# Kernel tuning notes

Measured on AMD Instinct MI355X. Metric: run time of the kernel, lower is better.

Reference implementation:

```python
import jax, jax.numpy as jnp
import numpy as np

NUM_HEADS = 16
ROPE_THETA = 10000.0


def _rope_tables(S, d_k):
    # angles[s, j] = s / theta^(2j/d_k), j over d_k/2 pairs
    inv_freq = 1.0 / (ROPE_THETA ** (jnp.arange(0, d_k, 2, dtype=jnp.float32) / d_k))
    angles = jnp.arange(S, dtype=jnp.float32)[:, None] * inv_freq[None, :]  # [S, d_k/2]
    # repeat_interleave(…, 2, dim=-1) -> [S, d_k]
    cos2 = jnp.repeat(jnp.cos(angles), 2, axis=-1)
    sin2 = jnp.repeat(jnp.sin(angles), 2, axis=-1)
    return cos2, sin2


def _rotate_half(x):
    x_even = x[..., 0::2]
    x_odd = x[..., 1::2]
    return jnp.stack([-x_odd, x_even], axis=-1).reshape(x.shape)


def _apply_rope(x, cos2, sin2):
    # x: [B, H, S, d_k]; cos2/sin2: [S, d_k] broadcast over B, H
    return x * cos2 + _rotate_half(x) * sin2


def setup_inputs() -> dict:
    key = jax.random.key(0)
    k1, k2, k3, k4, k5 = jax.random.split(key, 5)
    B, S, D = 2, 2048, 1024
    std = (2.0 / (D + D)) ** 0.5
    x = jax.random.normal(k1, (B, S, D), dtype=jnp.float32)
    Wq = jax.random.normal(k2, (D, D), dtype=jnp.float32) * std
    Wk = jax.random.normal(k3, (D, D), dtype=jnp.float32) * std
    Wv = jax.random.normal(k4, (D, D), dtype=jnp.float32) * std
    Wo = jax.random.normal(k5, (D, D), dtype=jnp.float32) * std
    return {"x": x, "Wq": Wq, "Wk": Wk, "Wv": Wv, "Wo": Wo}


def reference(x, Wq, Wk, Wv, Wo):
    B, S, D = x.shape
    H = NUM_HEADS
    d_k = D // H
    # Linear is y = W x with W[d_out, d_in]
    Q = jnp.einsum('bsd,ed->bse', x, Wq).reshape(B, S, H, d_k).transpose(0, 2, 1, 3)
    K = jnp.einsum('bsd,ed->bse', x, Wk).reshape(B, S, H, d_k).transpose(0, 2, 1, 3)
    V = jnp.einsum('bsd,ed->bse', x, Wv).reshape(B, S, H, d_k).transpose(0, 2, 1, 3)
    cos2, sin2 = _rope_tables(S, d_k)
    Q = _apply_rope(Q, cos2, sin2)
    K = _apply_rope(K, cos2, sin2)
    scores = jnp.einsum('bhqd,bhkd->bhqk', Q, K) / jnp.sqrt(jnp.float32(d_k))
    causal = jnp.tril(jnp.ones((S, S), dtype=bool))
    scores = jnp.where(causal, scores, -jnp.inf)
    attn = jax.nn.softmax(scores, axis=-1)
    out = jnp.einsum('bhqk,bhkd->bhqd', attn, V)  # [B,H,S,d_k]
    out = out.transpose(0, 2, 1, 3).reshape(B, S, D)
    return jnp.einsum('bsd,ed->bse', out, Wo)
```

## Files before the change

### kernel.cpp

```cpp
#include <hip/hip_runtime.h>
#include <hip/hip_bf16.h>

typedef float f32x4 __attribute__((ext_vector_type(4)));
typedef __bf16 bf16x8 __attribute__((ext_vector_type(8)));

static constexpr int S  = 2048;
static constexpr int D  = 1024;
static constexpr int DK = 64;
static constexpr int KDIM = 1024;

#define AS1 __attribute__((address_space(1)))
#define AS3 __attribute__((address_space(3)))

__device__ __forceinline__ void glds16(const void* g, void* l) {
  __builtin_amdgcn_global_load_lds((const AS1 void*)g, (AS3 void*)l, 16, 0, 0);
}

__device__ __forceinline__ unsigned cvtpk(float lo, float hi) {
  unsigned r;
  asm("v_cvt_pk_bf16_f32 %0, %1, %2" : "=v"(r) : "v"(lo), "v"(hi));
  return r;
}

__device__ __forceinline__ void pl32swap(unsigned& a, unsigned& b) {
  asm("v_permlane32_swap_b32 %0, %1" : "+v"(a), "+v"(b));
}

__device__ __forceinline__ int kperm64(int k) {
  const int kf = k >> 4, hs = (k >> 2) & 3, r = k & 3;
  const bool inl = ((kf & 1) == (hs >> 1));
  const int h = inl ? hs : (hs ^ 2);
  const int j = inl ? r : (r + 4);
  return ((kf >> 1) << 5) + (h << 3) + j;
}

__global__ __launch_bounds__(256) void cvt4_kernel(const float* __restrict__ src,
                                                   __hip_bfloat16* __restrict__ dst,
                                                   int n4) {
  int i = blockIdx.x * 256 + threadIdx.x;
  if (i >= n4) return;
  float4 v = reinterpret_cast<const float4*>(src)[i];
  union { ushort4 u; __hip_bfloat16 h[4]; } o;
  o.h[0] = __float2bfloat16(v.x);
  o.h[1] = __float2bfloat16(v.y);
  o.h[2] = __float2bfloat16(v.z);
  o.h[3] = __float2bfloat16(v.w);
  reinterpret_cast<ushort4*>(dst)[i] = o.u;
}

__global__ __launch_bounds__(256) void rope_tab_kernel(float* __restrict__ cosT,
                                                       float* __restrict__ sinT) {
  int idx = blockIdx.x * 256 + threadIdx.x;
  int s = idx >> 5, fi = idx & 31;
  float invf = powf(10000.0f, -(float)(2 * fi) / 64.0f);
  float ang = (float)s * invf;
  cosT[idx] = cosf(ang);
  sinT[idx] = sinf(ang);
}

template <int MODE>
__global__ __launch_bounds__(256) void gemm_nt_kernel(
    const __hip_bfloat16* __restrict__ A,
    const __hip_bfloat16* __restrict__ Bw,
    float* __restrict__ Cf,
    __hip_bfloat16* __restrict__ Qr,
    __hip_bfloat16* __restrict__ Kr,
    __hip_bfloat16* __restrict__ Vt,
    const float* __restrict__ cosT,
    const float* __restrict__ sinT,
    int Ncols) {
  __shared__ __attribute__((aligned(16))) __hip_bfloat16 Asm[128 * 32];
  __shared__ __attribute__((aligned(16))) __hip_bfloat16 Bsm[128 * 32];
  const int tid = threadIdx.x;
  const int nbn = Ncols >> 7;
  const int bm = blockIdx.x / nbn;
  const int bn = blockIdx.x % nbn;
  const int m0 = bm << 7, n0 = bn << 7;
  const int lane = tid & 63;
  const int wid = tid >> 6;
  const int wm = wid >> 1, wn = wid & 1;
  const int r16 = lane & 15, hf = lane >> 4;

  f32x4 acc[4][4];
#pragma unroll
  for (int i = 0; i < 4; ++i)
#pragma unroll
    for (int j = 0; j < 4; ++j) acc[i][j] = (f32x4)0.0f;

  for (int k0 = 0; k0 < KDIM; k0 += 32) {
    __syncthreads();
#pragma unroll
    for (int i = 0; i < 2; ++i) {
      const int idx = i * 256 + tid;
      const int row = idx >> 2;
      const int cb = (idx & 3) << 4;
      glds16((const char*)A + ((size_t)(m0 + row) * KDIM + k0) * 2 + cb,
             (char*)Asm + idx * 16);
      glds16((const char*)Bw + ((size_t)(n0 + row) * KDIM + k0) * 2 + cb,
             (char*)Bsm + idx * 16);
    }
    __syncthreads();
    bf16x8 af[4], bfr[4];
#pragma unroll
    for (int mi = 0; mi < 4; ++mi)
      af[mi] = *(const bf16x8*)((const char*)Asm +
                                ((wm << 6) + (mi << 4) + r16) * 64 + hf * 16);
#pragma unroll
    for (int ni = 0; ni < 4; ++ni)
      bfr[ni] = *(const bf16x8*)((const char*)Bsm +
                                 ((wn << 6) + (ni << 4) + r16) * 64 + hf * 16);
#pragma unroll
    for (int mi = 0; mi < 4; ++mi)
#pragma unroll
      for (int ni = 0; ni < 4; ++ni)
        acc[mi][ni] = __builtin_amdgcn_mfma_f32_16x16x32_bf16(af[mi], bfr[ni],
                                                              acc[mi][ni], 0, 0, 0);
  }

  if constexpr (MODE == 0) {
#pragma unroll
    for (int mi = 0; mi < 4; ++mi) {
      const int rowb = m0 + (wm << 6) + (mi << 4) + (hf << 2);
#pragma unroll
      for (int ni = 0; ni < 4; ++ni) {
        const int col = n0 + (wn << 6) + (ni << 4) + r16;
#pragma unroll
        for (int r = 0; r < 4; ++r)
          Cf[(size_t)(rowb + r) * Ncols + col] = acc[mi][ni][r];
      }
    }
  } else {
    const int proj = n0 >> 10;
#pragma unroll
    for (int mi = 0; mi < 4; ++mi) {
      const int rowb = m0 + (wm << 6) + (mi << 4) + (hf << 2);
#pragma unroll
      for (int ni = 0; ni < 4; ++ni) {
        const int col = n0 + (wn << 6) + (ni << 4) + r16;
        const int ecol = col & 1023;
        const int h = ecol >> 6, dk = ecol & 63;
#pragma unroll
        for (int r = 0; r < 4; ++r) {
          float v = acc[mi][ni][r];
          const int row = rowb + r;
          const int b = row >> 11, s = row & 2047;
          if (proj < 2) {
            float p = __shfl_xor(v, 1, 64);
            const int fi = dk >> 1;
            const float c = cosT[(s << 5) + fi];
            const float sn = sinT[(s << 5) + fi];
            const float ov = v * c + ((dk & 1) ? p : -p) * sn;
            __hip_bfloat16* dst = (proj == 0) ? Qr : Kr;
            dst[((size_t)((b << 4) + h) * S + s) * DK + dk] = __float2bfloat16(ov);
          } else {
            const int sp = (s & ~63) | kperm64(s & 63);
            Vt[((size_t)((b << 4) + h) * DK + dk) * S + sp] = __float2bfloat16(v);
          }
        }
      }
    }
  }
}

__global__ __launch_bounds__(256) void attn_kernel(
    const __hip_bfloat16* __restrict__ Q,
    const __hip_bfloat16* __restrict__ Kr,
    const __hip_bfloat16* __restrict__ Vp,
    __hip_bfloat16* __restrict__ AO) {
  __shared__ __attribute__((aligned(16))) __hip_bfloat16 Ks[2][64 * 64];
  __shared__ __attribute__((aligned(16))) __hip_bfloat16 Vs[2][64 * 64];
  const int tid = threadIdx.x;
  const int lane = tid & 63, wid = tid >> 6;
  const int r16 = lane & 15, hf = lane >> 4;
  const bool hi32 = (lane >= 32);
  const int qt = 15 - (blockIdx.x >> 5);
  const int bh = blockIdx.x & 31;
  const __hip_bfloat16* Qh = Q + (size_t)bh * S * DK;
  const __hip_bfloat16* Kh = Kr + (size_t)bh * S * DK;
  const __hip_bfloat16* Vh = Vp + (size_t)bh * DK * S;

  const int qbase = (qt << 7) + (wid << 5);

  bf16x8 bq[2][2];
#pragma unroll
  for (int qf = 0; qf < 2; ++qf)
#pragma unroll
    for (int ks = 0; ks < 2; ++ks)
      bq[qf][ks] = *(const bf16x8*)(Qh + (size_t)(qbase + (qf << 4) + r16) * DK +
                                    ks * 32 + hf * 8);

  f32x4 o[2][4];
#pragma unroll
  for (int qf = 0; qf < 2; ++qf)
#pragma unroll
    for (int f = 0; f < 4; ++f) o[qf][f] = (f32x4)0.0f;
  float m[2] = {-1e30f, -1e30f}, l[2] = {0.0f, 0.0f};

  const int nt = (qt << 1) + 2;

#define STAGE(bufi, t)                                                         \
  {                                                                            \
    _Pragma("unroll") for (int i = 0; i < 2; ++i) {                            \
      const int idx = i * 256 + tid;                                           \
      const int row = idx >> 3;                                                \
      const int cb = (idx & 7) << 4;                                           \
      const int scb = cb ^ ((row & 7) << 4);                                   \
      glds16((const char*)Kh + ((size_t)(((t) << 6) + row) * DK) * 2 + scb,    \
             (char*)(&Ks[bufi][0]) + idx * 16);                                \
      glds16((const char*)Vh + ((size_t)row * S + ((t) << 6)) * 2 + scb,       \
             (char*)(&Vs[bufi][0]) + idx * 16);                                \
    }                                                                          \
  }

  STAGE(0, 0);
  __syncthreads();

  for (int kt = 0; kt < nt; ++kt) {
    const int cur = kt & 1;
    if (kt + 1 < nt) STAGE(cur ^ 1, kt + 1);

    f32x4 p[2][4];
#pragma unroll
    for (int qf = 0; qf < 2; ++qf)
#pragma unroll
      for (int kf = 0; kf < 4; ++kf) p[qf][kf] = (f32x4)0.0f;
    __builtin_amdgcn_s_setprio(1);
#pragma unroll
    for (int ks = 0; ks < 2; ++ks) {
#pragma unroll
      for (int kf = 0; kf < 4; ++kf) {
        const int krow = (kf << 4) + r16;
        const int cb = (ks << 6) + (hf << 4);
        const bf16x8 ak = *(const bf16x8*)((const char*)(&Ks[cur][0]) +
                                           krow * 128 + (cb ^ ((krow & 7) << 4)));
#pragma unroll
        for (int qf = 0; qf < 2; ++qf)
          p[qf][kf] = __builtin_amdgcn_mfma_f32_16x16x32_bf16(ak, bq[qf][ks],
                                                              p[qf][kf], 0, 0, 0);
      }
    }
    __builtin_amdgcn_s_setprio(0);

    const bool diag = (kt >= (qt << 1));
#pragma unroll
    for (int qf = 0; qf < 2; ++qf) {
      const int qg = qbase + (qf << 4) + r16;
#pragma unroll
      for (int kf = 0; kf < 4; ++kf)
#pragma unroll
        for (int r = 0; r < 4; ++r) {
          float sv = p[qf][kf][r] * 0.125f;
          if (diag) {
            const int kg = (kt << 6) + (kf << 4) + (hf << 2) + r;
            if (kg > qg) sv = -1e30f;
          }
          p[qf][kf][r] = sv;
        }
    }

    float scl[2];
#pragma unroll
    for (int qf = 0; qf < 2; ++qf) {
      float t = p[qf][0][0];
#pragma unroll
      for (int kf = 0; kf < 4; ++kf)
#pragma unroll
        for (int r = 0; r < 4; ++r) t = fmaxf(t, p[qf][kf][r]);
      t = fmaxf(t, __shfl_xor(t, 16, 64));
      t = fmaxf(t, __shfl_xor(t, 32, 64));
      const float mn = fmaxf(m[qf], t);
      scl[qf] = __expf(m[qf] - mn);
      m[qf] = mn;
      float ss = 0.0f;
#pragma unroll
      for (int kf = 0; kf < 4; ++kf)
#pragma unroll
        for (int r = 0; r < 4; ++r) {
          const float e = __expf(p[qf][kf][r] - mn);
          p[qf][kf][r] = e;
          ss += e;
        }
      ss += __shfl_xor(ss, 16, 64);
      ss += __shfl_xor(ss, 32, 64);
      l[qf] = l[qf] * scl[qf] + ss;
#pragma unroll
      for (int f = 0; f < 4; ++f)
#pragma unroll
        for (int r = 0; r < 4; ++r) o[qf][f][r] *= scl[qf];
    }

    union PW { unsigned u[4]; bf16x8 v; };
    PW pb[2][2];
#pragma unroll
    for (int qf = 0; qf < 2; ++qf) {
      unsigned w[4][2];
#pragma unroll
      for (int kf = 0; kf < 4; ++kf) {
        w[kf][0] = cvtpk(p[qf][kf][0], p[qf][kf][1]);
        w[kf][1] = cvtpk(p[qf][kf][2], p[qf][kf][3]);
      }
#pragma unroll
      for (int ks = 0; ks < 2; ++ks) {
        unsigned a0 = w[2 * ks][0], b0 = w[2 * ks + 1][0];
        unsigned a1 = w[2 * ks][1], b1 = w[2 * ks + 1][1];
        pb[qf][ks].u[0] = hi32 ? b0 : a0;
        pb[qf][ks].u[1] = hi32 ? b1 : a1;
        pl32swap(a0, b0);
        pl32swap(a1, b1);
        pb[qf][ks].u[2] = hi32 ? a0 : b0;
        pb[qf][ks].u[3] = hi32 ? a1 : b1;
      }
    }

    __builtin_amdgcn_s_setprio(1);
#pragma unroll
    for (int ks = 0; ks < 2; ++ks) {
#pragma unroll
      for (int f = 0; f < 4; ++f) {
        const int vrow = (f << 4) + r16;
        const int cb = (ks << 6) + (hf << 4);
        const bf16x8 av = *(const bf16x8*)((const char*)(&Vs[cur][0]) +
                                           vrow * 128 + (cb ^ ((vrow & 7) << 4)));
#pragma unroll
        for (int qf = 0; qf < 2; ++qf)
          o[qf][f] = __builtin_amdgcn_mfma_f32_16x16x32_bf16(av, pb[qf][ks].v,
                                                             o[qf][f], 0, 0, 0);
      }
    }
    __builtin_amdgcn_s_setprio(0);

    __syncthreads();
  }
#undef STAGE

  const int b = bh >> 4, h = bh & 15;
#pragma unroll
  for (int qf = 0; qf < 2; ++qf) {
    const float inv = 1.0f / l[qf];
    const int q = qbase + (qf << 4) + r16;
#pragma unroll
    for (int f = 0; f < 4; ++f)
#pragma unroll
      for (int r = 0; r < 4; ++r) {
        const int dv = (f << 4) + (hf << 2) + r;
        AO[((size_t)b * S + q) * D + (h << 6) + dv] =
            __float2bfloat16(o[qf][f][r] * inv);
      }
  }
}

extern "C" void kernel_launch(void* const* d_in, const int* in_sizes, int n_in,
                              void* d_out, int out_size, void* d_ws, size_t ws_size,
                              hipStream_t stream) {
  (void)in_sizes; (void)n_in; (void)out_size; (void)ws_size;
  const float* x  = (const float*)d_in[0];
  const float* Wq = (const float*)d_in[1];
  const float* Wk = (const float*)d_in[2];
  const float* Wv = (const float*)d_in[3];
  const float* Wo = (const float*)d_in[4];
  float* out = (float*)d_out;
  char* ws = (char*)d_ws;
  const size_t MB = (size_t)1 << 20;
  __hip_bfloat16* xb   = (__hip_bfloat16*)(ws);
  __hip_bfloat16* Wcat = (__hip_bfloat16*)(ws + 8 * MB);
  __hip_bfloat16* Wob  = (__hip_bfloat16*)(ws + 14 * MB);
  __hip_bfloat16* Qr   = (__hip_bfloat16*)(ws + 16 * MB);
  __hip_bfloat16* Kr   = (__hip_bfloat16*)(ws + 24 * MB);
  __hip_bfloat16* Vt   = (__hip_bfloat16*)(ws + 32 * MB);
  __hip_bfloat16* AO   = (__hip_bfloat16*)(ws + 40 * MB);
  float* cosT = (float*)(ws + 48 * MB);
  float* sinT = (float*)(ws + 48 * MB + 256 * 1024);

  cvt4_kernel<<<4096, 256, 0, stream>>>(x, xb, (2 * 2048 * 1024) / 4);
  cvt4_kernel<<<1024, 256, 0, stream>>>(Wq, Wcat, (1024 * 1024) / 4);
  cvt4_kernel<<<1024, 256, 0, stream>>>(Wk, Wcat + 1024 * 1024, (1024 * 1024) / 4);
  cvt4_kernel<<<1024, 256, 0, stream>>>(Wv, Wcat + 2 * 1024 * 1024, (1024 * 1024) / 4);
  cvt4_kernel<<<1024, 256, 0, stream>>>(Wo, Wob, (1024 * 1024) / 4);
  rope_tab_kernel<<<(2048 * 32) / 256, 256, 0, stream>>>(cosT, sinT);

  gemm_nt_kernel<1><<<(4096 / 128) * (3072 / 128), 256, 0, stream>>>(
      xb, Wcat, nullptr, Qr, Kr, Vt, cosT, sinT, 3072);
  attn_kernel<<<32 * 16, 256, 0, stream>>>(Qr, Kr, Vt, AO);
  gemm_nt_kernel<0><<<(4096 / 128) * (1024 / 128), 256, 0, stream>>>(
      AO, Wob, out, nullptr, nullptr, nullptr, nullptr, nullptr, 1024);
}
```

Before: 230.6 us.

## Split long causal attention rows across blocks, fuse preprocessing, swizzle GEMM blocks

Attention work is rebalanced. The eight longest query tiles per head have their KV range split into two halves, each run as its own block, and the eight shorter tiles run whole. The split halves write normalized partial outputs plus (m, l) statistics into reused workspace, and a new merge kernel combines them. The goal is to cut the tail imbalance of the causal triangle. The five conversion launches and the RoPE-table launch are fused into one pre kernel to save launch overhead. GEMM block indices are remapped in an XCD-style interleave to improve L2 locality. Risks are the extra launch and partial-output traffic for the merge, and correctness of the merge if m is kept in a scaled domain.

Result: faster. 221.6 us (-3.9%).

```diff
diff --git a/kernel.cpp b/kernel.cpp
--- a/kernel.cpp
+++ b/kernel.cpp
@@ -34,28 +34,38 @@
   return ((kf >> 1) << 5) + (h << 3) + j;
 }
 
-__global__ __launch_bounds__(256) void cvt4_kernel(const float* __restrict__ src,
-                                                   __hip_bfloat16* __restrict__ dst,
-                                                   int n4) {
-  int i = blockIdx.x * 256 + threadIdx.x;
-  if (i >= n4) return;
-  float4 v = reinterpret_cast<const float4*>(src)[i];
-  union { ushort4 u; __hip_bfloat16 h[4]; } o;
-  o.h[0] = __float2bfloat16(v.x);
-  o.h[1] = __float2bfloat16(v.y);
-  o.h[2] = __float2bfloat16(v.z);
-  o.h[3] = __float2bfloat16(v.w);
-  reinterpret_cast<ushort4*>(dst)[i] = o.u;
-}
-
-__global__ __launch_bounds__(256) void rope_tab_kernel(float* __restrict__ cosT,
-                                                       float* __restrict__ sinT) {
-  int idx = blockIdx.x * 256 + threadIdx.x;
-  int s = idx >> 5, fi = idx & 31;
-  float invf = powf(10000.0f, -(float)(2 * fi) / 64.0f);
-  float ang = (float)s * invf;
-  cosT[idx] = cosf(ang);
-  sinT[idx] = sinf(ang);
+__global__ __launch_bounds__(256) void pre_kernel(
+    const float* __restrict__ x,  const float* __restrict__ Wq,
+    const float* __restrict__ Wk, const float* __restrict__ Wv,
+    const float* __restrict__ Wo,
+    __hip_bfloat16* __restrict__ xb, __hip_bfloat16* __restrict__ Wcat,
+    __hip_bfloat16* __restrict__ Wob,
+    float* __restrict__ cosT, float* __restrict__ sinT) {
+  const int gid = blockIdx.x * 256 + threadIdx.x;
+  if (gid < 2097152) {
+    const float* src;
+    __hip_bfloat16* dst;
+    int off;
+    if (gid < 1048576)      { src = x;  dst = xb;                  off = gid; }
+    else if (gid < 1310720) { src = Wq; dst = Wcat;                off = gid - 1048576; }
+    else if (gid < 1572864) { src = Wk; dst = Wcat + 1048576;      off = gid - 1310720; }
+    else if (gid < 1835008) { src = Wv; dst = Wcat + 2097152;      off = gid - 1572864; }
+    else                    { src = Wo; dst = Wob;                 off = gid - 1835008; }
+    float4 v = reinterpret_cast<const float4*>(src)[off];
+    union { ushort4 u; __hip_bfloat16 h[4]; } o;
+    o.h[0] = __float2bfloat16(v.x);
+    o.h[1] = __float2bfloat16(v.y);
+    o.h[2] = __float2bfloat16(v.z);
+    o.h[3] = __float2bfloat16(v.w);
+    reinterpret_cast<ushort4*>(dst)[off] = o.u;
+  } else {
+    const int idx = gid - 2097152;
+    const int s = idx >> 5, fi = idx & 31;
+    float invf = powf(10000.0f, -(float)(2 * fi) / 64.0f);
+    float ang = (float)s * invf;
+    cosT[idx] = cosf(ang);
+    sinT[idx] = sinf(ang);
+  }
 }
 
 template <int MODE>
@@ -73,8 +83,10 @@
   __shared__ __attribute__((aligned(16))) __hip_bfloat16 Bsm[128 * 32];
   const int tid = threadIdx.x;
   const int nbn = Ncols >> 7;
-  const int bm = blockIdx.x / nbn;
-  const int bn = blockIdx.x % nbn;
+  const int cpx = gridDim.x >> 3;
+  const int swz = (blockIdx.x & 7) * cpx + (blockIdx.x >> 3);
+  const int bm = swz / nbn;
+  const int bn = swz % nbn;
   const int m0 = bm << 7, n0 = bn << 7;
   const int lane = tid & 63;
   const int wid = tid >> 6;
@@ -166,15 +178,32 @@
     const __hip_bfloat16* __restrict__ Q,
     const __hip_bfloat16* __restrict__ Kr,
     const __hip_bfloat16* __restrict__ Vp,
-    __hip_bfloat16* __restrict__ AO) {
+    __hip_bfloat16* __restrict__ AO,
+    __hip_bfloat16* __restrict__ Opart,
+    float* __restrict__ ml) {
   __shared__ __attribute__((aligned(16))) __hip_bfloat16 Ks[2][64 * 64];
   __shared__ __attribute__((aligned(16))) __hip_bfloat16 Vs[2][64 * 64];
   const int tid = threadIdx.x;
   const int lane = tid & 63, wid = tid >> 6;
   const int r16 = lane & 15, hf = lane >> 4;
   const bool hi32 = (lane >= 32);
-  const int qt = 15 - (blockIdx.x >> 5);
   const int bh = blockIdx.x & 31;
+  const int item = blockIdx.x >> 5;
+  const int g = item / 3, j = item - 3 * g;
+  int qt, k0, k1;
+  bool dosplit;
+  if (j < 2) {
+    qt = 15 - g;
+    const int nt = (qt << 1) + 2;
+    k0 = j ? (nt >> 1) : 0;
+    k1 = j ? nt : (nt >> 1);
+    dosplit = true;
+  } else {
+    qt = 7 - g;
+    k0 = 0;
+    k1 = (qt << 1) + 2;
+    dosplit = false;
+  }
   const __hip_bfloat16* Qh = Q + (size_t)bh * S * DK;
   const __hip_bfloat16* Kh = Kr + (size_t)bh * S * DK;
   const __hip_bfloat16* Vh = Vp + (size_t)bh * DK * S;
@@ -195,8 +224,6 @@
 #pragma unroll
     for (int f = 0; f < 4; ++f) o[qf][f] = (f32x4)0.0f;
   float m[2] = {-1e30f, -1e30f}, l[2] = {0.0f, 0.0f};
-
-  const int nt = (qt << 1) + 2;
 
 #define STAGE(bufi, t)                                                         \
   {                                                                            \
@@ -212,12 +239,12 @@
     }                                                                          \
   }
 
-  STAGE(0, 0);
+  STAGE(0, k0);
   __syncthreads();
 
-  for (int kt = 0; kt < nt; ++kt) {
-    const int cur = kt & 1;
-    if (kt + 1 < nt) STAGE(cur ^ 1, kt + 1);
+  for (int kt = k0; kt < k1; ++kt) {
+    const int cur = (kt - k0) & 1;
+    if (kt + 1 < k1) STAGE(cur ^ 1, kt + 1);
 
     f32x4 p[2][4];
 #pragma unroll
@@ -333,19 +360,74 @@
   }
 #undef STAGE
 
+  if (!dosplit) {
+    const int b = bh >> 4, h = bh & 15;
+#pragma unroll
+    for (int qf = 0; qf < 2; ++qf) {
+      const float inv = 1.0f / l[qf];
+      const int q = qbase + (qf << 4) + r16;
+#pragma unroll
+      for (int f = 0; f < 4; ++f)
+#pragma unroll
+        for (int r = 0; r < 4; ++r) {
+          const int dv = (f << 4) + (hf << 2) + r;
+          AO[((size_t)b * S + q) * D + (h << 6) + dv] =
+              __float2bfloat16(o[qf][f][r] * inv);
+        }
+    }
+  } else {
+    const int sidx = (g << 1) | j;
+    __hip_bfloat16* op = Opart + (((size_t)bh * 16 + sidx) << 13);
+    float* mlp = ml + (((size_t)bh * 16 + sidx) << 8);
+#pragma unroll
+    for (int qf = 0; qf < 2; ++qf) {
+      const float inv = 1.0f / l[qf];
+      const int rowin = (wid << 5) + (qf << 4) + r16;
+#pragma unroll
+      for (int f = 0; f < 4; ++f)
+#pragma unroll
+        for (int r = 0; r < 4; ++r) {
+          const int dv = (f << 4) + (hf << 2) + r;
+          op[rowin * 64 + dv] = __float2bfloat16(o[qf][f][r] * inv);
+        }
+      if (hf == 0) {
+        mlp[rowin * 2] = m[qf];
+        mlp[rowin * 2 + 1] = l[qf];
+      }
+    }
+  }
+}
+
+__global__ __launch_bounds__(256) void merge_kernel(
+    const __hip_bfloat16* __restrict__ Opart,
+    const float* __restrict__ ml,
+    __hip_bfloat16* __restrict__ AO) {
+  const int rg = blockIdx.x * 256 + threadIdx.x;
+  const int bh = rg >> 10;
+  const int rem = rg & 1023;
+  const int gq = rem >> 7;
+  const int rowin = rem & 127;
+  const int s0 = bh * 16 + (gq << 1), s1 = s0 + 1;
+  const float m0 = ml[(s0 << 8) + rowin * 2], l0 = ml[(s0 << 8) + rowin * 2 + 1];
+  const float m1 = ml[(s1 << 8) + rowin * 2], l1 = ml[(s1 << 8) + rowin * 2 + 1];
+  const float mx = fmaxf(m0, m1);
+  float w0 = l0 * __expf(m0 - mx), w1 = l1 * __expf(m1 - mx);
+  const float inv = 1.0f / (w0 + w1);
+  w0 *= inv;
+  w1 *= inv;
+  const bf16x8* p0 = (const bf16x8*)(Opart + (((size_t)s0) << 13) + rowin * 64);
+  const bf16x8* p1 = (const bf16x8*)(Opart + (((size_t)s1) << 13) + rowin * 64);
   const int b = bh >> 4, h = bh & 15;
-#pragma unroll
-  for (int qf = 0; qf < 2; ++qf) {
-    const float inv = 1.0f / l[qf];
-    const int q = qbase + (qf << 4) + r16;
-#pragma unroll
-    for (int f = 0; f < 4; ++f)
-#pragma unroll
-      for (int r = 0; r < 4; ++r) {
-        const int dv = (f << 4) + (hf << 2) + r;
-        AO[((size_t)b * S + q) * D + (h << 6) + dv] =
-            __float2bfloat16(o[qf][f][r] * inv);
-      }
+  const int q = ((15 - gq) << 7) + rowin;
+  bf16x8* dst = (bf16x8*)(AO + ((size_t)b * S + q) * D + (h << 6));
+#pragma unroll
+  for (int i = 0; i < 8; ++i) {
+    bf16x8 a = p0[i], c = p1[i];
+    bf16x8 r;
+#pragma unroll
+    for (int e = 0; e < 8; ++e)
+      r[e] = (__bf16)(w0 * (float)a[e] + w1 * (float)c[e]);
+    dst[i] = r;
   }
 }
 
@@ -370,17 +452,15 @@
   __hip_bfloat16* AO   = (__hip_bfloat16*)(ws + 40 * MB);
   float* cosT = (float*)(ws + 48 * MB);
   float* sinT = (float*)(ws + 48 * MB + 256 * 1024);
-
-  cvt4_kernel<<<4096, 256, 0, stream>>>(x, xb, (2 * 2048 * 1024) / 4);
-  cvt4_kernel<<<1024, 256, 0, stream>>>(Wq, Wcat, (1024 * 1024) / 4);
-  cvt4_kernel<<<1024, 256, 0, stream>>>(Wk, Wcat + 1024 * 1024, (1024 * 1024) / 4);
-  cvt4_kernel<<<1024, 256, 0, stream>>>(Wv, Wcat + 2 * 1024 * 1024, (1024 * 1024) / 4);
-  cvt4_kernel<<<1024, 256, 0, stream>>>(Wo, Wob, (1024 * 1024) / 4);
-  rope_tab_kernel<<<(2048 * 32) / 256, 256, 0, stream>>>(cosT, sinT);
-
+  __hip_bfloat16* Opart = (__hip_bfloat16*)(ws);
+  float* mlbuf = (float*)(ws + 8 * MB);
+
+  pre_kernel<<<8448, 256, 0, stream>>>(x, Wq, Wk, Wv, Wo, xb, Wcat, Wob,
+                                       cosT, sinT);
   gemm_nt_kernel<1><<<(4096 / 128) * (3072 / 128), 256, 0, stream>>>(
       xb, Wcat, nullptr, Qr, Kr, Vt, cosT, sinT, 3072);
-  attn_kernel<<<32 * 16, 256, 0, stream>>>(Qr, Kr, Vt, AO);
+  attn_kernel<<<32 * 24, 256, 0, stream>>>(Qr, Kr, Vt, AO, Opart, mlbuf);
+  merge_kernel<<<128, 256, 0, stream>>>(Opart, mlbuf, AO);
   gemm_nt_kernel<0><<<(4096 / 128) * (1024 / 128), 256, 0, stream>>>(
       AO, Wob, out, nullptr, nullptr, nullptr, nullptr, nullptr, 1024);
 }
```
